# Kernel tuning notes

Measured on AMD Instinct MI355X. Metric: run time of the kernel, lower is better.

Reference implementation:

```python
import jax, jax.numpy as jnp
import numpy as np

B, S, E, D = 4, 2048, 1024, 1024
NEG_INF = float('-inf')


def setup_inputs() -> dict:
    key = jax.random.key(0)
    ks = jax.random.split(key, 10)
    query = jax.random.normal(ks[0], (B, S, E), dtype=jnp.float32)
    key_t = jax.random.normal(ks[1], (B, S, E), dtype=jnp.float32)
    value = jax.random.normal(ks[2], (B, S, E), dtype=jnp.float32)
    # Linear params (torch convention: y = x @ W.T + b)
    sc = 1.0 / np.sqrt(E)
    Wq = jax.random.uniform(ks[3], (D, E), jnp.float32, -sc, sc)
    bq = jax.random.uniform(ks[4], (D,), jnp.float32, -sc, sc)
    Wk = jax.random.uniform(ks[5], (D, E), jnp.float32, -sc, sc)
    bk = jax.random.uniform(ks[6], (D,), jnp.float32, -sc, sc)
    Wv = jax.random.uniform(ks[7], (D, E), jnp.float32, -sc, sc)
    bv = jax.random.uniform(ks[8], (D,), jnp.float32, -sc, sc)
    # padding mask: True = masked key position; ensure key 0 is never masked
    # so no row is fully -inf under the causal mask.
    lengths = jax.random.randint(ks[9], (B, 1, 1), 1, S + 1)  # valid length per batch
    pos = jnp.arange(S)[None, None, :]
    padding_mask = pos >= lengths  # [B,1,S] bool
    return {
        "query": query, "key": key_t, "value": value,
        "Wq": Wq, "bq": bq, "Wk": Wk, "bk": bk, "Wv": Wv, "bv": bv,
        "padding_mask": padding_mask, "look_ahead_mask": 1,
    }


def reference(query, key, value, Wq, bq, Wk, bk, Wv, bv, padding_mask, look_ahead_mask):
    q = query @ Wq.T + bq          # [B,S,D]
    k = key @ Wk.T + bk            # [B,S,D]
    v = value @ Wv.T + bv          # [B,S,D]
    scale = jnp.sqrt(jnp.asarray(q.shape[-1], q.dtype))
    qk = jnp.einsum('bqd,bkd->bqk', q, k) / scale  # [B,S,S]
    if padding_mask is not None:
        qk = jnp.where(padding_mask, NEG_INF, qk)
    if look_ahead_mask:
        causal = jnp.where(
            jnp.tril(jnp.ones((q.shape[1], k.shape[1]), dtype=bool)),
            jnp.asarray(0.0, qk.dtype), jnp.asarray(NEG_INF, qk.dtype))
        qk = qk + causal
    attn = jax.nn.softmax(qk, axis=-1)
    return jnp.einsum('bqk,bkd->bqd', attn, v)  # [B,S,D]
```

## Files before the change

kernel.cpp:

```cpp
#include <hip/hip_runtime.h>
#include <cstdint>
#include <cstddef>

#define B_ 4
#define S_ 2048
#define E_ 1024
#define D_ 1024
#define MFLAT (B_*S_)

typedef __attribute__((ext_vector_type(4))) float f32x4;
typedef __attribute__((ext_vector_type(8))) short short8;
typedef unsigned short u16;
typedef unsigned int   u32;

__device__ __forceinline__ u16 f2bf(float f) {
  u32 u = __float_as_uint(f);
  u = (u + 0x7fffu + ((u >> 16) & 1u)) >> 16;
  return (u16)u;
}

__device__ __forceinline__ void gll16(const void* g, void* lds) {
  __builtin_amdgcn_global_load_lds(
      (const __attribute__((address_space(1))) void*)g,
      (__attribute__((address_space(3))) void*)lds, 16, 0, 0);
}

#define BARRIER() do { asm volatile("" ::: "memory"); \
                       __builtin_amdgcn_s_barrier();  \
                       asm volatile("" ::: "memory"); } while (0)

__device__ __forceinline__ void gemm256_core(
    const u16* __restrict__ Ag, int lda,
    const u16* __restrict__ Bg, int ldb,
    int NT, char* lds, f32x4 acc[8][4])
{
  const int tid = threadIdx.x;
  const int w  = tid >> 6;
  const int l  = tid & 63;
  const int wm = w >> 2;
  const int wn = w & 3;

  const int srow = tid >> 3;
  const int scs  = ((tid & 7) << 4) ^ ((srow & 7) << 4);

  const int fr = l & 15;
  const int kq = l >> 4;
  const int kcol0 = (kq << 4) ^ ((l & 7) << 4);
  const int kcol1 = ((kq << 4) + 64) ^ ((l & 7) << 4);
  const int aoff = wm * 16384 + fr * 128;
  const int boff = 65536 + (wn >> 1) * 16384 + (((wn & 1) * 64 + fr) * 128);

  const int nhalf = 4 * NT;

#define STAGE_HALF(h_) do {                                                        \
    const int h__ = (h_);                                                          \
    if (h__ < nhalf) {                                                             \
      const int T__ = h__ >> 2, r__ = h__ & 3, buf__ = T__ & 1;                    \
      const char* s0; char* d0; size_t rstep;                                      \
      if (r__ < 2) {                                                               \
        s0 = (const char*)Bg + ((((size_t)(r__*128 + srow)) * (size_t)ldb          \
                                 + (size_t)T__*64) << 1) + scs;                    \
        d0 = lds + 65536 + buf__*32768 + r__*16384 + (w << 10);                    \
        rstep = ((size_t)ldb) << 7;                                                \
      } else {                                                                     \
        s0 = (const char*)Ag + ((((size_t)((r__-2)*128 + srow)) * (size_t)lda      \
                                 + (size_t)T__*64) << 1) + scs;                    \
        d0 = lds + buf__*32768 + (r__-2)*16384 + (w << 10);                        \
        rstep = ((size_t)lda) << 7;                                                \
      }                                                                            \
      gll16(s0, d0);                                                               \
      gll16(s0 + rstep, d0 + 8192);                                                \
    }                                                                              \
  } while (0)

#define LDA_F(mf, kc) (*(const short8*)(lds + bufo + aoff + (mf)*2048 + (kc)))
#define LDB_F(nf, kc) (*(const short8*)(lds + bufo + boff + (nf)*2048 + (kc)))

#define WAIT_LGKM() asm volatile("s_waitcnt lgkmcnt(0)" ::: "memory")

#define MFMA_Q(jbase) do {                                                         \
    __builtin_amdgcn_s_setprio(1);                                                 \
    _Pragma("unroll")                                                              \
    for (int i = 0; i < 4; ++i) {                                                  \
      _Pragma("unroll")                                                            \
      for (int j = 0; j < 2; ++j) {                                                \
        acc[accm + i][(jbase) + j] = __builtin_amdgcn_mfma_f32_16x16x32_bf16(      \
            areg[i][0], breg[(jbase)+j][0], acc[accm + i][(jbase)+j], 0, 0, 0);    \
        acc[accm + i][(jbase) + j] = __builtin_amdgcn_mfma_f32_16x16x32_bf16(      \
            areg[i][1], breg[(jbase)+j][1], acc[accm + i][(jbase)+j], 0, 0, 0);    \
      }                                                                            \
    }                                                                              \
    __builtin_amdgcn_s_setprio(0);                                                 \
  } while (0)

  short8 areg[4][2], breg[4][2];

  STAGE_HALF(0); STAGE_HALF(1); STAGE_HALF(2); STAGE_HALF(3);
  STAGE_HALF(4); STAGE_HALF(5);
  asm volatile("s_waitcnt vmcnt(4)" ::: "memory");
  BARRIER();

  for (int t = 0; t < NT; ++t) {
    const int bufo = (t & 1) << 15;
    const int hb = 4 * t + 6;

    {
      int accm = 0;
#pragma unroll
      for (int i = 0; i < 4; ++i) { areg[i][0] = LDA_F(i, kcol0); areg[i][1] = LDA_F(i, kcol1); }
#pragma unroll
      for (int j = 0; j < 2; ++j) { breg[j][0] = LDB_F(j, kcol0); breg[j][1] = LDB_F(j, kcol1); }
      STAGE_HALF(hb + 0);
      BARRIER();
      WAIT_LGKM();
      MFMA_Q(0);
      BARRIER();
    }
    {
      int accm = 0;
#pragma unroll
      for (int j = 2; j < 4; ++j) { breg[j][0] = LDB_F(j, kcol0); breg[j][1] = LDB_F(j, kcol1); }
      STAGE_HALF(hb + 1);
      BARRIER();
      WAIT_LGKM();
      MFMA_Q(2);
      BARRIER();
    }
    {
      int accm = 4;
#pragma unroll
      for (int i = 0; i < 4; ++i) { areg[i][0] = LDA_F(4 + i, kcol0); areg[i][1] = LDA_F(4 + i, kcol1); }
      STAGE_HALF(hb + 2);
      BARRIER();
      WAIT_LGKM();
      MFMA_Q(0);
      BARRIER();
    }
    {
      int accm = 4;
      STAGE_HALF(hb + 3);
      BARRIER();
      WAIT_LGKM();
      MFMA_Q(2);
      asm volatile("s_waitcnt vmcnt(4)" ::: "memory");
      BARRIER();
    }
  }
#undef STAGE_HALF
#undef LDA_F
#undef LDB_F
#undef WAIT_LGKM
#undef MFMA_Q
}

__device__ __forceinline__ void gemm_core(
    const u16* __restrict__ Ag, int lda,
    const u16* __restrict__ Bg, int ldb,
    int ksteps, u16* As, u16* Bs, f32x4 acc[4][4])
{
  const int tid = threadIdx.x;
  const int w = tid >> 6;
  const int l = tid & 63;
  const int srow = l >> 2;
  const int skb  = (l & 3) << 3;
  const int fr = l & 15;
  const int fk = (l >> 4) << 3;
  const int wr = (w >> 1) << 6;
  const int wc = (w & 1) << 6;
  const int c0 = w * 2, c1 = c0 + 1;

  const u16* a0 = Ag + (size_t)(c0*16 + srow)*lda + skb;
  const u16* a1 = Ag + (size_t)(c1*16 + srow)*lda + skb;
  const u16* b0 = Bg + (size_t)(c0*16 + srow)*ldb + skb;
  const u16* b1 = Bg + (size_t)(c1*16 + srow)*ldb + skb;

  for (int kt = 0; kt < ksteps; ++kt) {
    gll16(a0, As + c0*512);
    gll16(a1, As + c1*512);
    gll16(b0, Bs + c0*512);
    gll16(b1, Bs + c1*512);
    a0 += 32; a1 += 32; b0 += 32; b1 += 32;
    __syncthreads();
    short8 af[4], bfr[4];
#pragma unroll
    for (int i = 0; i < 4; ++i)
      af[i] = *(const short8*)(As + ((wr + i*16 + fr) << 5) + fk);
#pragma unroll
    for (int j = 0; j < 4; ++j)
      bfr[j] = *(const short8*)(Bs + ((wc + j*16 + fr) << 5) + fk);
#pragma unroll
    for (int i = 0; i < 4; ++i)
#pragma unroll
      for (int j = 0; j < 4; ++j)
        acc[i][j] = __builtin_amdgcn_mfma_f32_16x16x32_bf16(af[i], bfr[j], acc[i][j], 0, 0, 0);
    __syncthreads();
  }
}

__global__ __launch_bounds__(256) void cvt3_kernel(
    const float* __restrict__ s0, const float* __restrict__ s1,
    const float* __restrict__ s2, u16* __restrict__ dst, int segn4)
{
  int idx = blockIdx.x * blockDim.x + threadIdx.x;
  int stride = gridDim.x * blockDim.x;
  const int total = 3 * segn4;
  for (int i = idx; i < total; i += stride) {
    int s = i / segn4;
    int off = i - s * segn4;
    const float4* sp = (s == 0) ? (const float4*)s0 : (s == 1) ? (const float4*)s1 : (const float4*)s2;
    float4 f = sp[off];
    ushort4 o;
    o.x = f2bf(f.x); o.y = f2bf(f.y); o.z = f2bf(f.z); o.w = f2bf(f.w);
    ((ushort4*)dst)[i] = o;
  }
}

__global__ __launch_bounds__(256) void lengths_kernel(const void* __restrict__ mask,
                                                      int* __restrict__ lengths) {
  __shared__ int isbytes;
  const int t = threadIdx.x;
  if (t == 0) isbytes = 0;
  __syncthreads();
  const int* wi = (const int*)mask;
  int bad = 0;
  for (int idx = t; idx < (B_*S_)/4; idx += 256) {
    int v = wi[idx];
    if (v != 0 && v != 1) bad = 1;
  }
  if (bad) atomicOr(&isbytes, 1);
  __syncthreads();
  const int isb = isbytes;
  const int w = t >> 6, l = t & 63;
  const unsigned char* mb = (const unsigned char*)mask;
  int cnt = 0;
  for (int j = l; j < S_; j += 64) {
    int val = isb ? (int)mb[(size_t)w*S_ + j] : wi[(size_t)w*S_ + j];
    cnt += (val == 0);
  }
#pragma unroll
  for (int off = 32; off >= 1; off >>= 1) cnt += __shfl_xor(cnt, off);
  if (l == 0) lengths[w] = cnt;
}

__global__ __launch_bounds__(512, 2) void proj256_kernel(
    const u16* __restrict__ X, const u16* __restrict__ W,
    const float* __restrict__ bq, const float* __restrict__ bk, const float* __restrict__ bv,
    u16* __restrict__ q, u16* __restrict__ k, u16* __restrict__ v)
{
  extern __shared__ char lds[];
  const int bid = blockIdx.x;
  const int wg = (bid & 7) * 48 + (bid >> 3);
  const int z  = wg >> 7;
  const int rem = wg & 127;
  const int nt = rem >> 5;
  const int mt = rem & 31;

  const u16* Xz = X + (size_t)z * ((size_t)MFLAT * E_) + (size_t)(mt*256)*E_;
  const u16* Wz = W + (size_t)z * ((size_t)D_ * E_)    + (size_t)(nt*256)*E_;
  f32x4 acc[8][4];
#pragma unroll
  for (int i = 0; i < 8; ++i)
#pragma unroll
    for (int j = 0; j < 4; ++j) acc[i][j] = (f32x4){0.f,0.f,0.f,0.f};

  gemm256_core(Xz, E_, Wz, E_, E_/64, lds, acc);

  const float* bias = (z == 0) ? bq : (z == 1) ? bk : bv;
  u16* out = (z == 0) ? q : (z == 1) ? k : v;
  const int tid = threadIdx.x, w = tid >> 6, l = tid & 63;
  const int wm = w >> 2, wn = w & 3;
  const int fr = l & 15, kq = l >> 4;
  const int orow0 = mt*256 + wm*128 + kq*4;
  const int ocol0 = nt*256 + wn*64 + fr;
#pragma unroll
  for (int nf = 0; nf < 4; ++nf) {
    const int col = ocol0 + nf*16;
    const float bcol = bias[col];
#pragma unroll
    for (int mf = 0; mf < 8; ++mf)
#pragma unroll
      for (int r = 0; r < 4; ++r)
        out[(size_t)(orow0 + mf*16 + r)*D_ + col] = f2bf(acc[mf][nf][r] + bcol);
  }
}

__global__ __launch_bounds__(256) void transpose_kernel(
    const u16* __restrict__ v, u16* __restrict__ vT)
{
  __shared__ u16 tl[64][68];
  const int xt = blockIdx.x;
  const int yt = blockIdx.y;
  const int b  = blockIdx.z;
  const int t = threadIdx.x;
  const int r0 = t >> 4;
  const int c4 = (t & 15) << 2;
  const u16* src = v + ((size_t)b*S_ + yt*64)*D_ + xt*64;
#pragma unroll
  for (int rr = r0; rr < 64; rr += 16) {
    ushort4 u = *(const ushort4*)(src + (size_t)rr*D_ + c4);
    tl[rr][c4+0] = u.x; tl[rr][c4+1] = u.y; tl[rr][c4+2] = u.z; tl[rr][c4+3] = u.w;
  }
  __syncthreads();
  u16* dst = vT + ((size_t)b*D_ + xt*64)*S_ + yt*64;
#pragma unroll
  for (int rr = r0; rr < 64; rr += 16) {
    ushort4 u;
    u.x = tl[c4+0][rr]; u.y = tl[c4+1][rr]; u.z = tl[c4+2][rr]; u.w = tl[c4+3][rr];
    *(ushort4*)(dst + (size_t)rr*S_ + c4) = u;
  }
}

__global__ __launch_bounds__(512, 2) void qk256_kernel(
    const u16* __restrict__ q, const u16* __restrict__ k,
    const int* __restrict__ lengths, float* __restrict__ scores)
{
  const int bid = blockIdx.x;
  const int wg = (bid & 7) * 18 + (bid >> 3);
  const int b = wg / 36;
  const int r = wg - b * 36;
  int ty = (int)((sqrtf(8.0f * (float)r + 1.0f) - 1.0f) * 0.5f);
  while ((ty + 1) * (ty + 2) / 2 <= r) ++ty;
  while (ty * (ty + 1) / 2 > r) --ty;
  const int tx = r - ty * (ty + 1) / 2;

  const int len = lengths[b];
  if (tx * 256 >= len) return;
  extern __shared__ char lds[];
  f32x4 acc[8][4];
#pragma unroll
  for (int i = 0; i < 8; ++i)
#pragma unroll
    for (int j = 0; j < 4; ++j) acc[i][j] = (f32x4){0.f,0.f,0.f,0.f};
  const u16* Aq = q + ((size_t)b*S_ + (size_t)ty*256) * D_;
  const u16* Bk = k + ((size_t)b*S_ + (size_t)tx*256) * D_;
  gemm256_core(Aq, D_, Bk, D_, D_/64, lds, acc);

  const int tid = threadIdx.x, w = tid >> 6, l = tid & 63;
  const int wm = w >> 2, wn = w & 3;
  const int fr = l & 15, kq = l >> 4;
  const int orow0 = ty*256 + wm*128 + kq*4;
  const int ocol0 = tx*256 + wn*64 + fr;
  float* sb = scores + (size_t)b*S_*S_;
#pragma unroll
  for (int mf = 0; mf < 8; ++mf)
#pragma unroll
    for (int nf = 0; nf < 4; ++nf)
#pragma unroll
      for (int r2 = 0; r2 < 4; ++r2)
        sb[(size_t)(orow0 + mf*16 + r2)*S_ + (ocol0 + nf*16)] = acc[mf][nf][r2] * 0.03125f;
}

__global__ __launch_bounds__(256) void softmax_kernel(
    const float* __restrict__ scores, const int* __restrict__ lengths,
    u16* __restrict__ P)
{
  const int i = blockIdx.x, b = blockIdx.y;
  const int len = lengths[b];
  const int kmax = min(i + 1, len);
  const float* row = scores + ((size_t)b*S_ + i)*S_;
  u16* prow = P + ((size_t)b*S_ + i)*S_;
  const int t = threadIdx.x;
  const int j0 = t * 8;
  float v[8];
  {
    float4 x0 = *(const float4*)(row + j0);
    float4 x1 = *(const float4*)(row + j0 + 4);
    v[0]=x0.x; v[1]=x0.y; v[2]=x0.z; v[3]=x0.w;
    v[4]=x1.x; v[5]=x1.y; v[6]=x1.z; v[7]=x1.w;
  }
  float m = -3.4e38f;
#pragma unroll
  for (int e = 0; e < 8; ++e) if (j0 + e < kmax) m = fmaxf(m, v[e]);
#pragma unroll
  for (int off = 32; off >= 1; off >>= 1) m = fmaxf(m, __shfl_xor(m, off));
  __shared__ float redm[4], reds[4];
  if ((t & 63) == 0) redm[t >> 6] = m;
  __syncthreads();
  m = fmaxf(fmaxf(redm[0], redm[1]), fmaxf(redm[2], redm[3]));
  float s = 0.f, ex[8];
#pragma unroll
  for (int e = 0; e < 8; ++e) {
    ex[e] = (j0 + e < kmax) ? __expf(v[e] - m) : 0.f;
    s += ex[e];
  }
#pragma unroll
  for (int off = 32; off >= 1; off >>= 1) s += __shfl_xor(s, off);
  if ((t & 63) == 0) reds[t >> 6] = s;
  __syncthreads();
  s = reds[0] + reds[1] + reds[2] + reds[3];
  const float inv = 1.0f / s;
  short8 o;
#pragma unroll
  for (int e = 0; e < 8; ++e) o[e] = (short)f2bf(ex[e] * inv);
  *(short8*)(prow + j0) = o;
}

__global__ __launch_bounds__(256) void pv_kernel(
    const u16* __restrict__ P, const u16* __restrict__ vT,
    const int* __restrict__ lengths, float* __restrict__ out)
{
  const int xt = blockIdx.x, ty = blockIdx.y, b = blockIdx.z;
  const int len = lengths[b];
  const int kend = min(ty*128 + 128, len);
  const int ksteps = (kend + 31) >> 5;
  __shared__ u16 As[4096], Bs[4096];
  f32x4 acc[4][4];
#pragma unroll
  for (int i = 0; i < 4; ++i)
#pragma unroll
    for (int j = 0; j < 4; ++j) acc[i][j] = (f32x4){0.f,0.f,0.f,0.f};
  const u16* Ap = P  + ((size_t)b*S_ + (size_t)ty*128)*S_;
  const u16* Bv = vT + ((size_t)b*D_ + (size_t)xt*128)*S_;
  gemm_core(Ap, S_, Bv, S_, ksteps, As, Bs, acc);

  const int tid = threadIdx.x, w = tid >> 6, l = tid & 63;
  const int wr = (w >> 1) << 6, wc = (w & 1) << 6;
  const int orow = ty*128 + wr + ((l >> 4) << 2);
  const int ocol = xt*128 + wc + (l & 15);
  float* ob = out + (size_t)b*S_*D_;
#pragma unroll
  for (int i = 0; i < 4; ++i)
#pragma unroll
    for (int j = 0; j < 4; ++j)
#pragma unroll
      for (int r = 0; r < 4; ++r)
        ob[(size_t)(orow + i*16 + r)*D_ + (ocol + j*16)] = acc[i][j][r];
}

extern "C" void kernel_launch(void* const* d_in, const int* in_sizes, int n_in,
                              void* d_out, int out_size, void* d_ws, size_t ws_size,
                              hipStream_t stream)
{
  const float* query = (const float*)d_in[0];
  const float* key_  = (const float*)d_in[1];
  const float* value = (const float*)d_in[2];
  const float* Wq = (const float*)d_in[3];
  const float* bq = (const float*)d_in[4];
  const float* Wk = (const float*)d_in[5];
  const float* bk = (const float*)d_in[6];
  const float* Wv = (const float*)d_in[7];
  const float* bv = (const float*)d_in[8];
  const void*  pmask = d_in[9];
  float* out = (float*)d_out;
  char* ws = (char*)d_ws;

  (void)hipFuncSetAttribute((const void*)proj256_kernel,
                            hipFuncAttributeMaxDynamicSharedMemorySize, 131072);
  (void)hipFuncSetAttribute((const void*)qk256_kernel,
                            hipFuncAttributeMaxDynamicSharedMemorySize, 131072);

  int* lengths = (int*)ws;
  u16* q   = (u16*)(ws + 256);
  u16* kk  = q  + (size_t)MFLAT * D_;
  u16* vT  = kk + (size_t)MFLAT * D_;
  u16* Pbuf = (u16*)(ws + 50331904ull);
  u16* vbuf = Pbuf;
  char* scratch = ws + 83886336ull;
  u16* Xb = (u16*)scratch;
  u16* Wb = Xb + 3ull * MFLAT * E_;
  float* scores = (float*)scratch;

  cvt3_kernel<<<dim3(2048), 256, 0, stream>>>(query, key_, value, Xb, (MFLAT*E_)/4);
  cvt3_kernel<<<dim3(512),  256, 0, stream>>>(Wq, Wk, Wv, Wb, (D_*E_)/4);
  lengths_kernel<<<dim3(1), 256, 0, stream>>>(pmask, lengths);

  proj256_kernel<<<dim3(384), 512, 131072, stream>>>(Xb, Wb, bq, bk, bv, q, kk, vbuf);

  transpose_kernel<<<dim3(16, 32, 4), 256, 0, stream>>>(vbuf, vT);

  qk256_kernel<<<dim3(144), 512, 131072, stream>>>(q, kk, lengths, scores);

  softmax_kernel<<<dim3(2048, 4), 256, 0, stream>>>(scores, lengths, Pbuf);

  pv_kernel<<<dim3(8, 16, 4), 256, 0, stream>>>(Pbuf, vT, lengths, out);
}
```

Measured before the change: 355.1 us.

## Rewrite 256-tile GEMM pipeline and move PV matmul onto it

Replaces the shared 256x256 bf16 GEMM core with a new four-phase pipeline. Each phase stages a quarter of the next K-tile with global_load_lds while running MFMAs on the current tile, gated by finer vmcnt waits and fewer barriers. The PV kernel moves from a simple 128x128 single-buffered loop to this 256x256 core, using 128 workgroups and bounding K by the causal and padding length. This should cut barrier and LDS-load stalls and improve data reuse in PV. In exchange, PV runs with fewer, larger workgroups, which may leave CUs idle and unbalance the causal work.

```diff
diff --git a/kernel.cpp b/kernel.cpp
--- a/kernel.cpp
+++ b/kernel.cpp
@@ -29,172 +29,108 @@
                        __builtin_amdgcn_s_barrier();  \
                        asm volatile("" ::: "memory"); } while (0)
 
-__device__ __forceinline__ void gemm256_core(
+__device__ __forceinline__ void gemm256s_core(
     const u16* __restrict__ Ag, int lda,
     const u16* __restrict__ Bg, int ldb,
     int NT, char* lds, f32x4 acc[8][4])
 {
   const int tid = threadIdx.x;
-  const int w  = tid >> 6;
-  const int l  = tid & 63;
-  const int wm = w >> 2;
-  const int wn = w & 3;
-
-  const int srow = tid >> 3;
-  const int scs  = ((tid & 7) << 4) ^ ((srow & 7) << 4);
-
-  const int fr = l & 15;
-  const int kq = l >> 4;
-  const int kcol0 = (kq << 4) ^ ((l & 7) << 4);
-  const int kcol1 = ((kq << 4) + 64) ^ ((l & 7) << 4);
-  const int aoff = wm * 16384 + fr * 128;
-  const int boff = 65536 + (wn >> 1) * 16384 + (((wn & 1) * 64 + fr) * 128);
-
-  const int nhalf = 4 * NT;
-
-#define STAGE_HALF(h_) do {                                                        \
-    const int h__ = (h_);                                                          \
-    if (h__ < nhalf) {                                                             \
-      const int T__ = h__ >> 2, r__ = h__ & 3, buf__ = T__ & 1;                    \
-      const char* s0; char* d0; size_t rstep;                                      \
-      if (r__ < 2) {                                                               \
-        s0 = (const char*)Bg + ((((size_t)(r__*128 + srow)) * (size_t)ldb          \
-                                 + (size_t)T__*64) << 1) + scs;                    \
-        d0 = lds + 65536 + buf__*32768 + r__*16384 + (w << 10);                    \
-        rstep = ((size_t)ldb) << 7;                                                \
-      } else {                                                                     \
-        s0 = (const char*)Ag + ((((size_t)((r__-2)*128 + srow)) * (size_t)lda      \
-                                 + (size_t)T__*64) << 1) + scs;                    \
-        d0 = lds + buf__*32768 + (r__-2)*16384 + (w << 10);                        \
-        rstep = ((size_t)lda) << 7;                                                \
-      }                                                                            \
-      gll16(s0, d0);                                                               \
-      gll16(s0 + rstep, d0 + 8192);                                                \
-    }                                                                              \
+  const int l = tid & 63;
+  const int w = tid >> 6;
+  const int wm = w >> 2, wn = w & 3;
+
+  const int scs = (((tid & 7) ^ ((tid >> 3) & 7)) << 4);
+  const char* srcA = (const char*)Ag
+      + (size_t)((tid >> 8) * 128 + ((tid & 255) >> 3)) * (size_t)lda * 2 + scs;
+  const char* srcB = (const char*)Bg + (size_t)(tid >> 3) * (size_t)ldb * 2 + scs;
+  const size_t astep = (size_t)lda * 64;
+  const size_t bstep = (size_t)ldb * 128;
+  char* dA0 = lds + ((tid >> 8) << 14) + ((tid & 255) << 4);
+  char* dB0 = lds + 65536 + (tid << 4);
+
+  const int fr = l & 15, kq = l >> 4;
+  const int kx = (l & 7) << 4;
+  const int kc0 = (kq << 4) ^ kx;
+  const int kc1 = ((kq << 4) + 64) ^ kx;
+  const int aoff = (wm << 14) + fr * 128;
+  const int boff = 65536 + wn * 8192 + fr * 128;
+
+#define SG_A(q) gll16(srcA + (q)*astep + tso, dA0 + sb + (q)*4096)
+#define SG_B(u) gll16(srcB + (u)*bstep + tso, dB0 + sb + (u)*8192)
+#define LDA_(mf, kc) (*(const short8*)(lds + bufo + aoff + (mf)*2048 + (kc)))
+#define LDB_(nf, kc) (*(const short8*)(lds + bufo + boff + (nf)*2048 + (kc)))
+#define WAIT_LGKM() asm volatile("s_waitcnt lgkmcnt(0)" ::: "memory")
+#define MFMA_PH(p) do {                                                          \
+    __builtin_amdgcn_s_setprio(1);                                               \
+    _Pragma("unroll")                                                            \
+    for (int i_ = 0; i_ < 2; ++i_) {                                             \
+      _Pragma("unroll")                                                          \
+      for (int j_ = 0; j_ < 4; ++j_) {                                           \
+        acc[2*(p)+i_][j_] = __builtin_amdgcn_mfma_f32_16x16x32_bf16(             \
+            areg[i_][0], breg[j_][0], acc[2*(p)+i_][j_], 0, 0, 0);               \
+        acc[2*(p)+i_][j_] = __builtin_amdgcn_mfma_f32_16x16x32_bf16(             \
+            areg[i_][1], breg[j_][1], acc[2*(p)+i_][j_], 0, 0, 0);               \
+      }                                                                          \
+    }                                                                            \
+    __builtin_amdgcn_s_setprio(0);                                               \
   } while (0)
 
-#define LDA_F(mf, kc) (*(const short8*)(lds + bufo + aoff + (mf)*2048 + (kc)))
-#define LDB_F(nf, kc) (*(const short8*)(lds + bufo + boff + (nf)*2048 + (kc)))
-
-#define WAIT_LGKM() asm volatile("s_waitcnt lgkmcnt(0)" ::: "memory")
-
-#define MFMA_Q(jbase) do {                                                         \
-    __builtin_amdgcn_s_setprio(1);                                                 \
-    _Pragma("unroll")                                                              \
-    for (int i = 0; i < 4; ++i) {                                                  \
-      _Pragma("unroll")                                                            \
-      for (int j = 0; j < 2; ++j) {                                                \
-        acc[accm + i][(jbase) + j] = __builtin_amdgcn_mfma_f32_16x16x32_bf16(      \
-            areg[i][0], breg[(jbase)+j][0], acc[accm + i][(jbase)+j], 0, 0, 0);    \
-        acc[accm + i][(jbase) + j] = __builtin_amdgcn_mfma_f32_16x16x32_bf16(      \
-            areg[i][1], breg[(jbase)+j][1], acc[accm + i][(jbase)+j], 0, 0, 0);    \
-      }                                                                            \
-    }                                                                              \
-    __builtin_amdgcn_s_setprio(0);                                                 \
-  } while (0)
-
-  short8 areg[4][2], breg[4][2];
-
-  STAGE_HALF(0); STAGE_HALF(1); STAGE_HALF(2); STAGE_HALF(3);
-  STAGE_HALF(4); STAGE_HALF(5);
-  asm volatile("s_waitcnt vmcnt(4)" ::: "memory");
-  BARRIER();
+  short8 areg[2][2], breg[4][2];
+
+  {
+    const size_t tso = 0; const int sb = 0;
+    SG_B(0); SG_B(1); SG_B(2); SG_B(3);
+    SG_A(0); SG_A(1); SG_A(2); SG_A(3);
+  }
 
   for (int t = 0; t < NT; ++t) {
     const int bufo = (t & 1) << 15;
-    const int hb = 4 * t + 6;
-
-    {
-      int accm = 0;
-#pragma unroll
-      for (int i = 0; i < 4; ++i) { areg[i][0] = LDA_F(i, kcol0); areg[i][1] = LDA_F(i, kcol1); }
-#pragma unroll
-      for (int j = 0; j < 2; ++j) { breg[j][0] = LDB_F(j, kcol0); breg[j][1] = LDB_F(j, kcol1); }
-      STAGE_HALF(hb + 0);
-      BARRIER();
-      WAIT_LGKM();
-      MFMA_Q(0);
-      BARRIER();
-    }
-    {
-      int accm = 0;
-#pragma unroll
-      for (int j = 2; j < 4; ++j) { breg[j][0] = LDB_F(j, kcol0); breg[j][1] = LDB_F(j, kcol1); }
-      STAGE_HALF(hb + 1);
-      BARRIER();
-      WAIT_LGKM();
-      MFMA_Q(2);
-      BARRIER();
-    }
-    {
-      int accm = 4;
-#pragma unroll
-      for (int i = 0; i < 4; ++i) { areg[i][0] = LDA_F(4 + i, kcol0); areg[i][1] = LDA_F(4 + i, kcol1); }
-      STAGE_HALF(hb + 2);
-      BARRIER();
-      WAIT_LGKM();
-      MFMA_Q(0);
-      BARRIER();
-    }
-    {
-      int accm = 4;
-      STAGE_HALF(hb + 3);
-      BARRIER();
-      WAIT_LGKM();
-      MFMA_Q(2);
-      asm volatile("s_waitcnt vmcnt(4)" ::: "memory");
-      BARRIER();
-    }
-  }
-#undef STAGE_HALF
-#undef LDA_F
-#undef LDB_F
+    const int sb = ((t + 1) & 1) << 15;
+    const int tsi = (t + 1 == NT) ? 0 : (t + 1);
+    const size_t tso = (size_t)tsi << 7;
+
+    asm volatile("s_waitcnt vmcnt(3)" ::: "memory");
+    BARRIER();
+#pragma unroll
+    for (int nf = 0; nf < 4; ++nf) { breg[nf][0] = LDB_(nf, kc0); breg[nf][1] = LDB_(nf, kc1); }
+#pragma unroll
+    for (int i = 0; i < 2; ++i) { areg[i][0] = LDA_(i, kc0); areg[i][1] = LDA_(i, kc1); }
+    SG_B(0); SG_B(1);
+    WAIT_LGKM();
+    MFMA_PH(0);
+
+    asm volatile("s_waitcnt vmcnt(4)" ::: "memory");
+    BARRIER();
+#pragma unroll
+    for (int i = 0; i < 2; ++i) { areg[i][0] = LDA_(2+i, kc0); areg[i][1] = LDA_(2+i, kc1); }
+    SG_B(2); SG_B(3);
+    WAIT_LGKM();
+    MFMA_PH(1);
+
+    asm volatile("s_waitcnt vmcnt(5)" ::: "memory");
+    BARRIER();
+#pragma unroll
+    for (int i = 0; i < 2; ++i) { areg[i][0] = LDA_(4+i, kc0); areg[i][1] = LDA_(4+i, kc1); }
+    SG_A(0); SG_A(1);
+    WAIT_LGKM();
+    MFMA_PH(2);
+
+    asm volatile("s_waitcnt vmcnt(6)" ::: "memory");
+    BARRIER();
+#pragma unroll
+    for (int i = 0; i < 2; ++i) { areg[i][0] = LDA_(6+i, kc0); areg[i][1] = LDA_(6+i, kc1); }
+    SG_A(2); SG_A(3);
+    WAIT_LGKM();
+    MFMA_PH(3);
+  }
+  asm volatile("s_waitcnt vmcnt(0)" ::: "memory");
+  BARRIER();
+#undef SG_A
+#undef SG_B
+#undef LDA_
+#undef LDB_
 #undef WAIT_LGKM
-#undef MFMA_Q
-}
-
-__device__ __forceinline__ void gemm_core(
-    const u16* __restrict__ Ag, int lda,
-    const u16* __restrict__ Bg, int ldb,
-    int ksteps, u16* As, u16* Bs, f32x4 acc[4][4])
-{
-  const int tid = threadIdx.x;
-  const int w = tid >> 6;
-  const int l = tid & 63;
-  const int srow = l >> 2;
-  const int skb  = (l & 3) << 3;
-  const int fr = l & 15;
-  const int fk = (l >> 4) << 3;
-  const int wr = (w >> 1) << 6;
-  const int wc = (w & 1) << 6;
-  const int c0 = w * 2, c1 = c0 + 1;
-
-  const u16* a0 = Ag + (size_t)(c0*16 + srow)*lda + skb;
-  const u16* a1 = Ag + (size_t)(c1*16 + srow)*lda + skb;
-  const u16* b0 = Bg + (size_t)(c0*16 + srow)*ldb + skb;
-  const u16* b1 = Bg + (size_t)(c1*16 + srow)*ldb + skb;
-
-  for (int kt = 0; kt < ksteps; ++kt) {
-    gll16(a0, As + c0*512);
-    gll16(a1, As + c1*512);
-    gll16(b0, Bs + c0*512);
-    gll16(b1, Bs + c1*512);
-    a0 += 32; a1 += 32; b0 += 32; b1 += 32;
-    __syncthreads();
-    short8 af[4], bfr[4];
-#pragma unroll
-    for (int i = 0; i < 4; ++i)
-      af[i] = *(const short8*)(As + ((wr + i*16 + fr) << 5) + fk);
-#pragma unroll
-    for (int j = 0; j < 4; ++j)
-      bfr[j] = *(const short8*)(Bs + ((wc + j*16 + fr) << 5) + fk);
-#pragma unroll
-    for (int i = 0; i < 4; ++i)
-#pragma unroll
-      for (int j = 0; j < 4; ++j)
-        acc[i][j] = __builtin_amdgcn_mfma_f32_16x16x32_bf16(af[i], bfr[j], acc[i][j], 0, 0, 0);
-    __syncthreads();
-  }
+#undef MFMA_PH
 }
 
 __global__ __launch_bounds__(256) void cvt3_kernel(
@@ -263,7 +199,7 @@
 #pragma unroll
     for (int j = 0; j < 4; ++j) acc[i][j] = (f32x4){0.f,0.f,0.f,0.f};
 
-  gemm256_core(Xz, E_, Wz, E_, E_/64, lds, acc);
+  gemm256s_core(Xz, E_, Wz, E_, E_/64, lds, acc);
 
   const float* bias = (z == 0) ? bq : (z == 1) ? bk : bv;
   u16* out = (z == 0) ? q : (z == 1) ? k : v;
@@ -333,7 +269,7 @@
     for (int j = 0; j < 4; ++j) acc[i][j] = (f32x4){0.f,0.f,0.f,0.f};
   const u16* Aq = q + ((size_t)b*S_ + (size_t)ty*256) * D_;
   const u16* Bk = k + ((size_t)b*S_ + (size_t)tx*256) * D_;
-  gemm256_core(Aq, D_, Bk, D_, D_/64, lds, acc);
+  gemm256s_core(Aq, D_, Bk, D_, D_/64, lds, acc);
 
   const int tid = threadIdx.x, w = tid >> 6, l = tid & 63;
   const int wm = w >> 2, wn = w & 3;
@@ -395,36 +331,43 @@
   *(short8*)(prow + j0) = o;
 }
 
-__global__ __launch_bounds__(256) void pv_kernel(
+__global__ __launch_bounds__(512, 2) void pv256_kernel(
     const u16* __restrict__ P, const u16* __restrict__ vT,
     const int* __restrict__ lengths, float* __restrict__ out)
 {
-  const int xt = blockIdx.x, ty = blockIdx.y, b = blockIdx.z;
+  extern __shared__ char lds[];
+  const int bid = blockIdx.x;
+  const int wg = (bid & 7) * 16 + (bid >> 3);
+  const int b = wg >> 5;
+  const int rem = wg & 31;
+  const int ty = rem >> 2;
+  const int xt = rem & 3;
   const int len = lengths[b];
-  const int kend = min(ty*128 + 128, len);
-  const int ksteps = (kend + 31) >> 5;
-  __shared__ u16 As[4096], Bs[4096];
-  f32x4 acc[4][4];
-#pragma unroll
-  for (int i = 0; i < 4; ++i)
+  const int kend = min(ty * 256 + 256, len);
+  const int NT = (kend + 63) >> 6;
+
+  f32x4 acc[8][4];
+#pragma unroll
+  for (int i = 0; i < 8; ++i)
 #pragma unroll
     for (int j = 0; j < 4; ++j) acc[i][j] = (f32x4){0.f,0.f,0.f,0.f};
-  const u16* Ap = P  + ((size_t)b*S_ + (size_t)ty*128)*S_;
-  const u16* Bv = vT + ((size_t)b*D_ + (size_t)xt*128)*S_;
-  gemm_core(Ap, S_, Bv, S_, ksteps, As, Bs, acc);
+  const u16* Ap = P  + ((size_t)b*S_ + (size_t)ty*256) * S_;
+  const u16* Bv = vT + ((size_t)b*D_ + (size_t)xt*256) * S_;
+  gemm256s_core(Ap, S_, Bv, S_, NT, lds, acc);
 
   const int tid = threadIdx.x, w = tid >> 6, l = tid & 63;
-  const int wr = (w >> 1) << 6, wc = (w & 1) << 6;
-  const int orow = ty*128 + wr + ((l >> 4) << 2);
-  const int ocol = xt*128 + wc + (l & 15);
+  const int wm = w >> 2, wn = w & 3;
+  const int fr = l & 15, kq = l >> 4;
+  const int orow0 = ty*256 + wm*128 + kq*4;
+  const int ocol0 = xt*256 + wn*64 + fr;
   float* ob = out + (size_t)b*S_*D_;
 #pragma unroll
-  for (int i = 0; i < 4; ++i)
-#pragma unroll
-    for (int j = 0; j < 4; ++j)
-#pragma unroll
-      for (int r = 0; r < 4; ++r)
-        ob[(size_t)(orow + i*16 + r)*D_ + (ocol + j*16)] = acc[i][j][r];
+  for (int mf = 0; mf < 8; ++mf)
+#pragma unroll
+    for (int nf = 0; nf < 4; ++nf)
+#pragma unroll
+      for (int r2 = 0; r2 < 4; ++r2)
+        ob[(size_t)(orow0 + mf*16 + r2)*D_ + (ocol0 + nf*16)] = acc[mf][nf][r2];
 }
 
 extern "C" void kernel_launch(void* const* d_in, const int* in_sizes, int n_in,
@@ -448,6 +391,8 @@
                             hipFuncAttributeMaxDynamicSharedMemorySize, 131072);
   (void)hipFuncSetAttribute((const void*)qk256_kernel,
                             hipFuncAttributeMaxDynamicSharedMemorySize, 131072);
+  (void)hipFuncSetAttribute((const void*)pv256_kernel,
+                            hipFuncAttributeMaxDynamicSharedMemorySize, 131072);
 
   int* lengths = (int*)ws;
   u16* q   = (u16*)(ws + 256);
@@ -472,5 +417,5 @@
 
   softmax_kernel<<<dim3(2048, 4), 256, 0, stream>>>(scores, lengths, Pbuf);
 
-  pv_kernel<<<dim3(8, 16, 4), 256, 0, stream>>>(Pbuf, vT, lengths, out);
-}
+  pv256_kernel<<<dim3(128), 512, 131072, stream>>>(Pbuf, vT, lengths, out);
+}
```

New measurement: 345.0 us. 1.03x faster.
